# Optimization experiments

Measured on AMD Instinct MI355X. Metric: run time of the kernel, lower is better.

## Reference

```python
import jax, jax.numpy as jnp
import numpy as np
from jax.ops import segment_sum

N = 100000
E = 1600000
NFEAT, NHID, NCLS = 128, 64, 40


def setup_inputs() -> dict:
    key = jax.random.key(0)
    ks = jax.random.split(key, 8)
    x = jax.random.normal(ks[0], (N, NFEAT), dtype=jnp.float32)
    edge_index = jax.random.randint(ks[1], (2, E), 0, N, dtype=jnp.int64)
    s = lambda fi, fo: (2.0 / (fi + fo)) ** 0.5  # glorot-ish
    W1 = jax.random.normal(ks[2], (NFEAT, NHID), dtype=jnp.float32) * s(NFEAT, NHID)
    b1 = jnp.zeros((NHID,), dtype=jnp.float32)
    W2 = jax.random.normal(ks[3], (NHID, NHID), dtype=jnp.float32) * s(NHID, NHID)
    b2 = jnp.zeros((NHID,), dtype=jnp.float32)
    Wc = jax.random.normal(ks[4], (NHID, NCLS), dtype=jnp.float32) * s(NHID, NCLS)
    bc = jnp.zeros((NCLS,), dtype=jnp.float32)
    return {"x": x, "edge_index": edge_index, "W1": W1, "b1": b1,
            "W2": W2, "b2": b2, "Wc": Wc, "bc": bc}


def _gcn_conv(x, W, b, row, col, dinv):
    # x: [N, Fin] -> [N, Fout]; symmetric-normalized aggregation (PyG GCNConv)
    h = x @ W                                   # [N, Fout]
    norm = dinv[row] * dinv[col]                # [E+N]
    msg = h[row] * norm[:, None]                # [E+N, Fout]
    out = segment_sum(msg, col, num_segments=N) # [N, Fout]
    return out + b


def reference(x, edge_index, W1, b1, W2, b2, Wc, bc):
    # add self loops
    loops = jnp.arange(N, dtype=edge_index.dtype)
    row = jnp.concatenate([edge_index[0], loops])
    col = jnp.concatenate([edge_index[1], loops])
    # symmetric normalization degrees (edge weight = 1)
    deg = segment_sum(jnp.ones_like(col, dtype=x.dtype), col, num_segments=N)
    dinv = jnp.where(deg > 0, jax.lax.rsqrt(deg), 0.0)
    h = jax.nn.relu(_gcn_conv(x, W1, b1, row, col, dinv))
    h = jax.nn.relu(_gcn_conv(h, W2, b2, row, col, dinv))
    return h @ Wc + bc
```

## Files before the change

kernel.cpp:

```cpp
#include <hip/hip_runtime.h>

#define NN 100000
#define NE 1600000
#define NF 128
#define NH 64
#define NC 40

#define BKN 128
#define NBK ((NN + BKN - 1) / BKN)
#define CH  4096
#define NCHB ((NE + CH - 1) / CH)
#define CAPB 2560
#define OFFS (BKN + 1)
#define HCAP 1408
#define HTS 36

typedef short bf16x8 __attribute__((ext_vector_type(8)));
typedef float f32x4  __attribute__((ext_vector_type(4)));

__device__ __forceinline__ unsigned short f2bf(float f) {
    unsigned int u = __builtin_bit_cast(unsigned int, f);
    u += 0x7FFFu + ((u >> 16) & 1u);
    return (unsigned short)(u >> 16);
}
__device__ __forceinline__ float bfl(unsigned int u) {
    return __builtin_bit_cast(float, u << 16);
}
__device__ __forceinline__ float bfh(unsigned int u) {
    return __builtin_bit_cast(float, u & 0xFFFF0000u);
}
__device__ __forceinline__ unsigned int pk2(float a, float b) {
    return (unsigned int)f2bf(a) | ((unsigned int)f2bf(b) << 16);
}
__device__ __forceinline__ void bacc8(float4& lo, float4& hi, uint4 v) {
    lo.x += bfl(v.x); hi.x += bfh(v.x);
    lo.y += bfl(v.y); hi.y += bfh(v.y);
    lo.z += bfl(v.z); hi.z += bfh(v.z);
    lo.w += bfl(v.w); hi.w += bfh(v.w);
}

__global__ void zero_gcnt(int* __restrict__ g) {
    int i = blockIdx.x * 256 + threadIdx.x;
    if (i < NBK) g[i] = 0;
}

__global__ __launch_bounds__(256) void prep_wt(const float* __restrict__ W2,
                                               const float* __restrict__ Wc,
                                               unsigned short* __restrict__ Wt2,
                                               unsigned short* __restrict__ Wtc) {
    int t = blockIdx.x * 256 + threadIdx.x;
    if (t < 64 * 64) {
        int j = t >> 6, k = t & 63;
        Wt2[j * 64 + k] = f2bf(W2[k * 64 + j]);
    } else if (t < 64 * 64 + 48 * 64) {
        int u = t - 64 * 64;
        int j = u >> 6, k = u & 63;
        Wtc[j * 64 + k] = (j < NC) ? f2bf(Wc[k * NC + j]) : (unsigned short)0;
    }
}

__global__ __launch_bounds__(256) void bucket_scatter(const int* __restrict__ row,
                                                      const int* __restrict__ col,
                                                      int* __restrict__ gcnt,
                                                      unsigned int* __restrict__ encs) {
    __shared__ int h[NBK];
    __shared__ int loff[NBK];
    __shared__ int cur[NBK];
    __shared__ int gbase[NBK];
    __shared__ unsigned int stage[CH];
    __shared__ unsigned short sbkt[CH];
    int tid = threadIdx.x;
    for (int i = tid; i < NBK; i += 256) h[i] = 0;
    __syncthreads();
    int e0 = blockIdx.x * CH;
    int nval = NE - e0; if (nval > CH) nval = CH;
    int c[16];
    #pragma unroll
    for (int i = 0; i < 16; ++i) {
        int e = e0 + i * 256 + tid;
        c[i] = (e < NE) ? col[e] : -1;
        if (c[i] >= 0) atomicAdd(&h[c[i] >> 7], 1);
    }
    __syncthreads();
    if (tid < 64) {
        int lane = tid, base = lane * 13;
        int pre[13]; int sum = 0;
        #pragma unroll
        for (int j = 0; j < 13; ++j) {
            int idx = base + j;
            int x = (idx < NBK) ? h[idx] : 0;
            pre[j] = sum; sum += x;
        }
        int run = sum;
        #pragma unroll
        for (int d = 1; d < 64; d <<= 1) {
            int n = __shfl_up(run, d, 64);
            if (lane >= d) run += n;
        }
        int lex = run - sum;
        #pragma unroll
        for (int j = 0; j < 13; ++j) {
            int idx = base + j;
            if (idx < NBK) { loff[idx] = lex + pre[j]; cur[idx] = lex + pre[j]; }
        }
    }
    __syncthreads();
    for (int i = tid; i < NBK; i += 256) {
        int cnt = h[i];
        gbase[i] = cnt ? atomicAdd(&gcnt[i], cnt) : 0;
    }
    __syncthreads();
    #pragma unroll
    for (int i = 0; i < 16; ++i) {
        int e = e0 + i * 256 + tid;
        if (e < NE) {
            int cc = c[i], b = cc >> 7;
            int r = atomicAdd(&cur[b], 1);
            stage[r] = ((unsigned int)(cc & 127) << 24) | (unsigned int)row[e];
            sbkt[r] = (unsigned short)b;
        }
    }
    __syncthreads();
    for (int s = tid; s < nval; s += 256) {
        int b = sbkt[s];
        encs[(size_t)b * CAPB + gbase[b] + (s - loff[b])] = stage[s];
    }
}

__global__ __launch_bounds__(256) void csr_sort(unsigned int* __restrict__ encs,
                                                const int* __restrict__ gcnt,
                                                int* __restrict__ offg,
                                                float* __restrict__ dinv) {
    __shared__ unsigned int sseg[CAPB];
    __shared__ int h[BKN];
    __shared__ int off[OFFS];
    __shared__ int cur[BKN];
    int b = blockIdx.x, tid = threadIdx.x;
    if (tid < BKN) h[tid] = 0;
    __syncthreads();
    int m = gcnt[b];
    unsigned int* seg = encs + (size_t)b * CAPB;
    for (int s = tid; s < m; s += 256) {
        unsigned int e = seg[s];
        sseg[s] = e;
        atomicAdd(&h[e >> 24], 1);
    }
    __syncthreads();
    if (tid < BKN) {
        int g = b * BKN + tid;
        if (g < NN) dinv[g] = rsqrtf((float)(h[tid] + 1));
    }
    if (tid < 64) {
        int lane = tid;
        int x0 = h[lane * 2], x1 = h[lane * 2 + 1];
        int sum = x0 + x1, run = sum;
        #pragma unroll
        for (int d = 1; d < 64; d <<= 1) {
            int n = __shfl_up(run, d, 64);
            if (lane >= d) run += n;
        }
        int ex = run - sum;
        off[lane * 2] = ex;          cur[lane * 2] = ex;
        off[lane * 2 + 1] = ex + x0; cur[lane * 2 + 1] = ex + x0;
        if (lane == 63) off[BKN] = run;
    }
    __syncthreads();
    for (int s = tid; s < m; s += 256) {
        unsigned int e = sseg[s];
        int n = e >> 24;
        int r = atomicAdd(&cur[n], 1);
        seg[r] = e & 0xFFFFFFu;
    }
    if (tid < OFFS) offg[b * OFFS + tid] = off[tid];
}

template <int K, int N>
__global__ __launch_bounds__(256) void gemm_tiled(const float* __restrict__ X,
                                                  const float* __restrict__ W,
                                                  const float* __restrict__ aux,
                                                  unsigned short* __restrict__ hsb) {
    constexpr int KT  = 64;
    constexpr int KTP = KT + 4;
    __shared__ float Xl[64 * KTP];
    __shared__ float Wl[KT * N + 64];
    int tid = threadIdx.x;
    int tr = tid >> 4, tc = tid & 15;
    int rbase = blockIdx.x * 64;
    float4 acc[4] = {};

    for (int kt = 0; kt < K; kt += KT) {
        int fid = tid;
        #pragma unroll
        for (int p = 0; p < 4; ++p, fid += 256) {
            int m = fid >> 4, k4 = fid & 15;
            int rr = rbase + m; if (rr >= NN) rr = NN - 1;
            float4 v = *(const float4*)(X + (size_t)rr * K + kt + k4 * 4);
            *(float4*)(Xl + m * KTP + k4 * 4) = v;
        }
        constexpr int NW4 = KT * N / 4;
        for (int f = tid; f < NW4; f += 256)
            ((float4*)Wl)[f] = *((const float4*)(W + (size_t)kt * N) + f);
        __syncthreads();

        #pragma unroll 2
        for (int k4 = 0; k4 < KT / 4; ++k4) {
            float4 xa[4], wa[4];
            #pragma unroll
            for (int i = 0; i < 4; ++i)
                xa[i] = *(const float4*)(Xl + (tr * 4 + i) * KTP + k4 * 4);
            #pragma unroll
            for (int j = 0; j < 4; ++j)
                wa[j] = *(const float4*)(Wl + (k4 * 4 + j) * N + tc * 4);
            #pragma unroll
            for (int i = 0; i < 4; ++i) {
                acc[i].x = fmaf(xa[i].x, wa[0].x, acc[i].x);
                acc[i].y = fmaf(xa[i].x, wa[0].y, acc[i].y);
                acc[i].z = fmaf(xa[i].x, wa[0].z, acc[i].z);
                acc[i].w = fmaf(xa[i].x, wa[0].w, acc[i].w);
                acc[i].x = fmaf(xa[i].y, wa[1].x, acc[i].x);
                acc[i].y = fmaf(xa[i].y, wa[1].y, acc[i].y);
                acc[i].z = fmaf(xa[i].y, wa[1].z, acc[i].z);
                acc[i].w = fmaf(xa[i].y, wa[1].w, acc[i].w);
                acc[i].x = fmaf(xa[i].z, wa[2].x, acc[i].x);
                acc[i].y = fmaf(xa[i].z, wa[2].y, acc[i].y);
                acc[i].z = fmaf(xa[i].z, wa[2].z, acc[i].z);
                acc[i].w = fmaf(xa[i].z, wa[2].w, acc[i].w);
                acc[i].x = fmaf(xa[i].w, wa[3].x, acc[i].x);
                acc[i].y = fmaf(xa[i].w, wa[3].y, acc[i].y);
                acc[i].z = fmaf(xa[i].w, wa[3].z, acc[i].z);
                acc[i].w = fmaf(xa[i].w, wa[3].w, acc[i].w);
            }
        }
        __syncthreads();
    }

    #pragma unroll
    for (int i = 0; i < 4; ++i) {
        int r = rbase + tr * 4 + i;
        if (r < NN) {
            float d = aux[r];
            ushort4 o;
            o.x = f2bf(acc[i].x * d);
            o.y = f2bf(acc[i].y * d);
            o.z = f2bf(acc[i].z * d);
            o.w = f2bf(acc[i].w * d);
            *(ushort4*)(hsb + (size_t)r * N + tc * 4) = o;
        }
    }
}

template <int FINAL>
__global__ __launch_bounds__(256) void agg_matmul(const unsigned short* __restrict__ hs,
                                                  const int* __restrict__ srow,
                                                  const int* __restrict__ offg,
                                                  const float* __restrict__ dinv,
                                                  const float* __restrict__ biasA,
                                                  const unsigned short* __restrict__ Wt,
                                                  const float* __restrict__ biasB,
                                                  unsigned short* __restrict__ hsb_out,
                                                  float* __restrict__ f_out) {
    __shared__ int off[65];
    __shared__ int sidx[HCAP];
    __shared__ unsigned int htb[64 * HTS];
    __shared__ float sdinv[64];
    int b = blockIdx.x >> 1, half = blockIdx.x & 1;
    int tid = threadIdx.x;
    int rbase = b * BKN + half * 64;
    if (tid < 65) off[tid] = offg[b * OFFS + half * 64 + tid];
    __syncthreads();
    int e0 = off[0], cnt = off[64] - e0;
    const int* ptr = srow + (size_t)b * CAPB + e0;
    for (int s = tid; s < cnt; s += 256) sidx[s] = ptr[s];
    __syncthreads();

    int wid = tid >> 6, lane = tid & 63;
    int sg = lane >> 3, sl = lane & 7;
    const uint4* hs8 = (const uint4*)hs;
    #pragma unroll
    for (int k = 0; k < 2; ++k) {
        int n = k * 32 + wid * 8 + sg;
        int g = rbase + n;
        float d = (g < NN) ? dinv[g] : 0.f;
        if (sl == 0) sdinv[n] = d;
        float4 o0 = {}, o1 = {};
        if (g < NN) {
            float4 lo0 = {}, hi0 = {}, lo1 = {}, hi1 = {};
            float4 lo2 = {}, hi2 = {}, lo3 = {}, hi3 = {};
            bacc8(lo0, hi0, hs8[(size_t)g * 8 + sl]);
            int e = off[n] - e0, ee = off[n + 1] - e0;
            for (; e + 8 <= ee; e += 8) {
                int r0 = sidx[e + 0], r1 = sidx[e + 1];
                int r2 = sidx[e + 2], r3 = sidx[e + 3];
                int r4 = sidx[e + 4], r5 = sidx[e + 5];
                int r6 = sidx[e + 6], r7 = sidx[e + 7];
                uint4 v0 = hs8[(size_t)r0 * 8 + sl];
                uint4 v1 = hs8[(size_t)r1 * 8 + sl];
                uint4 v2 = hs8[(size_t)r2 * 8 + sl];
                uint4 v3 = hs8[(size_t)r3 * 8 + sl];
                uint4 v4 = hs8[(size_t)r4 * 8 + sl];
                uint4 v5 = hs8[(size_t)r5 * 8 + sl];
                uint4 v6 = hs8[(size_t)r6 * 8 + sl];
                uint4 v7 = hs8[(size_t)r7 * 8 + sl];
                bacc8(lo0, hi0, v0); bacc8(lo1, hi1, v1);
                bacc8(lo2, hi2, v2); bacc8(lo3, hi3, v3);
                bacc8(lo0, hi0, v4); bacc8(lo1, hi1, v5);
                bacc8(lo2, hi2, v6); bacc8(lo3, hi3, v7);
            }
            if (e + 4 <= ee) {
                int r0 = sidx[e + 0], r1 = sidx[e + 1];
                int r2 = sidx[e + 2], r3 = sidx[e + 3];
                uint4 v0 = hs8[(size_t)r0 * 8 + sl];
                uint4 v1 = hs8[(size_t)r1 * 8 + sl];
                uint4 v2 = hs8[(size_t)r2 * 8 + sl];
                uint4 v3 = hs8[(size_t)r3 * 8 + sl];
                bacc8(lo0, hi0, v0); bacc8(lo1, hi1, v1);
                bacc8(lo2, hi2, v2); bacc8(lo3, hi3, v3);
                e += 4;
            }
            for (; e < ee; ++e)
                bacc8(lo0, hi0, hs8[(size_t)sidx[e] * 8 + sl]);
            lo0.x += lo1.x + lo2.x + lo3.x;  hi0.x += hi1.x + hi2.x + hi3.x;
            lo0.y += lo1.y + lo2.y + lo3.y;  hi0.y += hi1.y + hi2.y + hi3.y;
            lo0.z += lo1.z + lo2.z + lo3.z;  hi0.z += hi1.z + hi2.z + hi3.z;
            lo0.w += lo1.w + lo2.w + lo3.w;  hi0.w += hi1.w + hi2.w + hi3.w;
            float4 bb0 = ((const float4*)biasA)[sl * 2];
            float4 bb1 = ((const float4*)biasA)[sl * 2 + 1];
            o0.x = fmaxf(fmaf(lo0.x, d, bb0.x), 0.f);
            o0.y = fmaxf(fmaf(hi0.x, d, bb0.y), 0.f);
            o0.z = fmaxf(fmaf(lo0.y, d, bb0.z), 0.f);
            o0.w = fmaxf(fmaf(hi0.y, d, bb0.w), 0.f);
            o1.x = fmaxf(fmaf(lo0.z, d, bb1.x), 0.f);
            o1.y = fmaxf(fmaf(hi0.z, d, bb1.y), 0.f);
            o1.z = fmaxf(fmaf(lo0.w, d, bb1.z), 0.f);
            o1.w = fmaxf(fmaf(hi0.w, d, bb1.w), 0.f);
        }
        uint4 pk;
        pk.x = pk2(o0.x, o0.y);
        pk.y = pk2(o0.z, o0.w);
        pk.z = pk2(o1.x, o1.y);
        pk.w = pk2(o1.z, o1.w);
        *(uint4*)&htb[n * HTS + sl * 4] = pk;
    }
    __syncthreads();

    constexpr int NCT = FINAL ? 3 : 4;
    int lm = lane & 15, lg = lane >> 4;
    bf16x8 afrag[2];
    #pragma unroll
    for (int kh = 0; kh < 2; ++kh) {
        const unsigned int* p = &htb[(wid * 16 + lm) * HTS + kh * 16 + lg * 4];
        afrag[kh] = __builtin_bit_cast(bf16x8, *(const uint4*)p);
    }
    f32x4 acc[NCT];
    #pragma unroll
    for (int ct = 0; ct < NCT; ++ct) {
        acc[ct] = (f32x4){0.f, 0.f, 0.f, 0.f};
        #pragma unroll
        for (int kh = 0; kh < 2; ++kh) {
            const unsigned short* q = Wt + (size_t)(ct * 16 + lm) * 64 + kh * 32 + lg * 8;
            bf16x8 bfrag = __builtin_bit_cast(bf16x8, *(const uint4*)q);
            acc[ct] = __builtin_amdgcn_mfma_f32_16x16x32_bf16(afrag[kh], bfrag, acc[ct], 0, 0, 0);
        }
    }

    if (!FINAL) {
        #pragma unroll
        for (int ct = 0; ct < NCT; ++ct) {
            #pragma unroll
            for (int rg = 0; rg < 4; ++rg) {
                int rloc = wid * 16 + lg * 4 + rg;
                int r = rbase + rloc;
                if (r < NN) {
                    float v = acc[ct][rg] * sdinv[rloc];
                    hsb_out[(size_t)r * NH + ct * 16 + lm] = f2bf(v);
                }
            }
        }
    } else {
        #pragma unroll
        for (int ct = 0; ct < NCT; ++ct) {
            int c = ct * 16 + lm;
            if (c < NC) {
                float bb = biasB[c];
                #pragma unroll
                for (int rg = 0; rg < 4; ++rg) {
                    int rloc = wid * 16 + lg * 4 + rg;
                    int r = rbase + rloc;
                    if (r < NN)
                        f_out[(size_t)r * NC + c] = acc[ct][rg] + bb;
                }
            }
        }
    }
}


extern "C" void kernel_launch(void* const* d_in, const int* in_sizes, int n_in,
                              void* d_out, int out_size, void* d_ws, size_t ws_size,
                              hipStream_t stream) {
    const float* x  = (const float*)d_in[0];
    const int* ei   = (const int*)d_in[1];
    const int* row  = ei;
    const int* col  = ei + NE;
    const float* W1 = (const float*)d_in[2];
    const float* b1 = (const float*)d_in[3];
    const float* W2 = (const float*)d_in[4];
    const float* b2 = (const float*)d_in[5];
    const float* Wc = (const float*)d_in[6];
    const float* bc = (const float*)d_in[7];
    float* out = (float*)d_out;

    char* ws = (char*)d_ws;
    size_t off = 0;
    auto alloc = [&](size_t bytes) {
        void* p = ws + off;
        off = (off + bytes + 255) & ~(size_t)255;
        return p;
    };
    int*   gcnt = (int*)alloc((size_t)NBK * 4);
    int*   offg = (int*)alloc((size_t)NBK * OFFS * 4);
    float* dinv = (float*)alloc((size_t)NN * 4);
    unsigned int* encs = (unsigned int*)alloc((size_t)NBK * CAPB * 4);
    unsigned short* hsb1 = (unsigned short*)alloc((size_t)NN * NH * 2);
    unsigned short* hsb2 = (unsigned short*)alloc((size_t)NN * NH * 2);
    unsigned short* Wt2  = (unsigned short*)alloc((size_t)64 * 64 * 2);
    unsigned short* Wtc  = (unsigned short*)alloc((size_t)48 * 64 * 2);

    const int GB = (NN + 63) / 64;

    zero_gcnt<<<(NBK + 255) / 256, 256, 0, stream>>>(gcnt);
    prep_wt<<<28, 256, 0, stream>>>(W2, Wc, Wt2, Wtc);
    bucket_scatter<<<NCHB, 256, 0, stream>>>(row, col, gcnt, encs);
    csr_sort<<<NBK, 256, 0, stream>>>(encs, gcnt, offg, dinv);

    gemm_tiled<NF, NH><<<GB, 256, 0, stream>>>(x, W1, dinv, hsb1);
    agg_matmul<0><<<NBK * 2, 256, 0, stream>>>(hsb1, (const int*)encs, offg, dinv,
                                               b1, Wt2, nullptr, hsb2, nullptr);
    agg_matmul<1><<<NBK * 2, 256, 0, stream>>>(hsb2, (const int*)encs, offg, dinv,
                                               b2, Wtc, bc, nullptr, out);
}
```

Measured before the change: 160.2 us.

## Use bf16 MFMA for first GEMM, widen aggregation blocks, fold zeroing into prep

Replaces the FP32 scalar-FMA tiled GEMM for layer 1 with a bf16 MFMA kernel that converts x to bf16 in shared memory and reads a pre-transposed bf16 W1. The aggregation kernels move from 256 to 512 threads so each thread handles one node/slot instead of looping twice, and the MFMA output tiles are split across 8 waves. The gcnt zeroing kernel is merged into the weight prep kernel, removing one launch. Converting x to bf16 before the first matmul lowers precision further.

After: 151.3 us. 5.6% less time.

```diff
diff --git a/kernel.cpp b/kernel.cpp
--- a/kernel.cpp
+++ b/kernel.cpp
@@ -14,6 +14,7 @@
 #define OFFS (BKN + 1)
 #define HCAP 1408
 #define HTS 36
+#define XTS 68
 
 typedef short bf16x8 __attribute__((ext_vector_type(8)));
 typedef float f32x4  __attribute__((ext_vector_type(4)));
@@ -39,23 +40,27 @@
     lo.w += bfl(v.w); hi.w += bfh(v.w);
 }
 
-__global__ void zero_gcnt(int* __restrict__ g) {
-    int i = blockIdx.x * 256 + threadIdx.x;
-    if (i < NBK) g[i] = 0;
-}
-
-__global__ __launch_bounds__(256) void prep_wt(const float* __restrict__ W2,
+__global__ __launch_bounds__(256) void prep_wt(const float* __restrict__ W1,
+                                               const float* __restrict__ W2,
                                                const float* __restrict__ Wc,
+                                               unsigned short* __restrict__ Wt1,
                                                unsigned short* __restrict__ Wt2,
-                                               unsigned short* __restrict__ Wtc) {
+                                               unsigned short* __restrict__ Wtc,
+                                               int* __restrict__ gcnt) {
     int t = blockIdx.x * 256 + threadIdx.x;
-    if (t < 64 * 64) {
-        int j = t >> 6, k = t & 63;
+    if (t < 8192) {
+        int j = t >> 7, k = t & 127;
+        Wt1[j * 128 + k] = f2bf(W1[k * 64 + j]);
+    } else if (t < 8192 + 4096) {
+        int u = t - 8192;
+        int j = u >> 6, k = u & 63;
         Wt2[j * 64 + k] = f2bf(W2[k * 64 + j]);
-    } else if (t < 64 * 64 + 48 * 64) {
-        int u = t - 64 * 64;
+    } else if (t < 8192 + 4096 + 3072) {
+        int u = t - 8192 - 4096;
         int j = u >> 6, k = u & 63;
         Wtc[j * 64 + k] = (j < NC) ? f2bf(Wc[k * NC + j]) : (unsigned short)0;
+    } else if (t < 8192 + 4096 + 3072 + NBK) {
+        gcnt[t - 8192 - 4096 - 3072] = 0;
     }
 }
 
@@ -174,83 +179,64 @@
     if (tid < OFFS) offg[b * OFFS + tid] = off[tid];
 }
 
-template <int K, int N>
-__global__ __launch_bounds__(256) void gemm_tiled(const float* __restrict__ X,
-                                                  const float* __restrict__ W,
-                                                  const float* __restrict__ aux,
+__global__ __launch_bounds__(256) void gemm1_mfma(const float* __restrict__ x,
+                                                  const unsigned short* __restrict__ Wt1,
+                                                  const float* __restrict__ dinv,
                                                   unsigned short* __restrict__ hsb) {
-    constexpr int KT  = 64;
-    constexpr int KTP = KT + 4;
-    __shared__ float Xl[64 * KTP];
-    __shared__ float Wl[KT * N + 64];
+    __shared__ unsigned int Xl[64 * XTS];
+    __shared__ float sdv[64];
     int tid = threadIdx.x;
-    int tr = tid >> 4, tc = tid & 15;
     int rbase = blockIdx.x * 64;
-    float4 acc[4] = {};
-
-    for (int kt = 0; kt < K; kt += KT) {
-        int fid = tid;
-        #pragma unroll
-        for (int p = 0; p < 4; ++p, fid += 256) {
-            int m = fid >> 4, k4 = fid & 15;
-            int rr = rbase + m; if (rr >= NN) rr = NN - 1;
-            float4 v = *(const float4*)(X + (size_t)rr * K + kt + k4 * 4);
-            *(float4*)(Xl + m * KTP + k4 * 4) = v;
-        }
-        constexpr int NW4 = KT * N / 4;
-        for (int f = tid; f < NW4; f += 256)
-            ((float4*)Wl)[f] = *((const float4*)(W + (size_t)kt * N) + f);
-        __syncthreads();
-
-        #pragma unroll 2
-        for (int k4 = 0; k4 < KT / 4; ++k4) {
-            float4 xa[4], wa[4];
-            #pragma unroll
-            for (int i = 0; i < 4; ++i)
-                xa[i] = *(const float4*)(Xl + (tr * 4 + i) * KTP + k4 * 4);
-            #pragma unroll
-            for (int j = 0; j < 4; ++j)
-                wa[j] = *(const float4*)(Wl + (k4 * 4 + j) * N + tc * 4);
-            #pragma unroll
-            for (int i = 0; i < 4; ++i) {
-                acc[i].x = fmaf(xa[i].x, wa[0].x, acc[i].x);
-                acc[i].y = fmaf(xa[i].x, wa[0].y, acc[i].y);
-                acc[i].z = fmaf(xa[i].x, wa[0].z, acc[i].z);
-                acc[i].w = fmaf(xa[i].x, wa[0].w, acc[i].w);
-                acc[i].x = fmaf(xa[i].y, wa[1].x, acc[i].x);
-                acc[i].y = fmaf(xa[i].y, wa[1].y, acc[i].y);
-                acc[i].z = fmaf(xa[i].y, wa[1].z, acc[i].z);
-                acc[i].w = fmaf(xa[i].y, wa[1].w, acc[i].w);
-                acc[i].x = fmaf(xa[i].z, wa[2].x, acc[i].x);
-                acc[i].y = fmaf(xa[i].z, wa[2].y, acc[i].y);
-                acc[i].z = fmaf(xa[i].z, wa[2].z, acc[i].z);
-                acc[i].w = fmaf(xa[i].z, wa[2].w, acc[i].w);
-                acc[i].x = fmaf(xa[i].w, wa[3].x, acc[i].x);
-                acc[i].y = fmaf(xa[i].w, wa[3].y, acc[i].y);
-                acc[i].z = fmaf(xa[i].w, wa[3].z, acc[i].z);
-                acc[i].w = fmaf(xa[i].w, wa[3].w, acc[i].w);
-            }
-        }
-        __syncthreads();
-    }
-
-    #pragma unroll
-    for (int i = 0; i < 4; ++i) {
-        int r = rbase + tr * 4 + i;
-        if (r < NN) {
-            float d = aux[r];
-            ushort4 o;
-            o.x = f2bf(acc[i].x * d);
-            o.y = f2bf(acc[i].y * d);
-            o.z = f2bf(acc[i].z * d);
-            o.w = f2bf(acc[i].w * d);
-            *(ushort4*)(hsb + (size_t)r * N + tc * 4) = o;
+    if (tid < 64) {
+        int r = rbase + tid;
+        sdv[tid] = (r < NN) ? dinv[r] : 0.f;
+    }
+    #pragma unroll
+    for (int p = 0; p < 8; ++p) {
+        int fid = p * 256 + tid;
+        int m = fid >> 5, c4 = fid & 31;
+        int rr = rbase + m; if (rr >= NN) rr = NN - 1;
+        float4 v = *(const float4*)(x + (size_t)rr * NF + c4 * 4);
+        uint2 u;
+        u.x = pk2(v.x, v.y);
+        u.y = pk2(v.z, v.w);
+        *(uint2*)&Xl[m * XTS + c4 * 2] = u;
+    }
+    __syncthreads();
+
+    int wid = tid >> 6, lane = tid & 63;
+    int lm = lane & 15, lg = lane >> 4;
+    int rt = wid;
+    bf16x8 af[4];
+    #pragma unroll
+    for (int kh = 0; kh < 4; ++kh)
+        af[kh] = __builtin_bit_cast(bf16x8,
+                    *(const uint4*)&Xl[(rt * 16 + lm) * XTS + kh * 16 + lg * 4]);
+    f32x4 acc[4];
+    #pragma unroll
+    for (int ct = 0; ct < 4; ++ct) {
+        acc[ct] = (f32x4){0.f, 0.f, 0.f, 0.f};
+        #pragma unroll
+        for (int kh = 0; kh < 4; ++kh) {
+            bf16x8 bf = __builtin_bit_cast(bf16x8,
+                *(const uint4*)(Wt1 + (size_t)(ct * 16 + lm) * 128 + kh * 32 + lg * 8));
+            acc[ct] = __builtin_amdgcn_mfma_f32_16x16x32_bf16(af[kh], bf, acc[ct], 0, 0, 0);
+        }
+    }
+    #pragma unroll
+    for (int ct = 0; ct < 4; ++ct) {
+        #pragma unroll
+        for (int rg = 0; rg < 4; ++rg) {
+            int rloc = rt * 16 + lg * 4 + rg;
+            int r = rbase + rloc;
+            if (r < NN)
+                hsb[(size_t)r * NH + ct * 16 + lm] = f2bf(acc[ct][rg] * sdv[rloc]);
         }
     }
 }
 
 template <int FINAL>
-__global__ __launch_bounds__(256) void agg_matmul(const unsigned short* __restrict__ hs,
+__global__ __launch_bounds__(512) void agg_matmul(const unsigned short* __restrict__ hs,
                                                   const int* __restrict__ srow,
                                                   const int* __restrict__ offg,
                                                   const float* __restrict__ dinv,
@@ -270,16 +256,13 @@
     __syncthreads();
     int e0 = off[0], cnt = off[64] - e0;
     const int* ptr = srow + (size_t)b * CAPB + e0;
-    for (int s = tid; s < cnt; s += 256) sidx[s] = ptr[s];
-    __syncthreads();
-
-    int wid = tid >> 6, lane = tid & 63;
-    int sg = lane >> 3, sl = lane & 7;
+    for (int s = tid; s < cnt; s += 512) sidx[s] = ptr[s];
+    __syncthreads();
+
+    int n = tid >> 3, sl = tid & 7;
+    int g = rbase + n;
     const uint4* hs8 = (const uint4*)hs;
-    #pragma unroll
-    for (int k = 0; k < 2; ++k) {
-        int n = k * 32 + wid * 8 + sg;
-        int g = rbase + n;
+    {
         float d = (g < NN) ? dinv[g] : 0.f;
         if (sl == 0) sdinv[n] = d;
         float4 o0 = {}, o1 = {};
@@ -344,50 +327,45 @@
     __syncthreads();
 
     constexpr int NCT = FINAL ? 3 : 4;
+    int wid = tid >> 6, lane = tid & 63;
     int lm = lane & 15, lg = lane >> 4;
+    int rt = wid >> 1;
+    int ct0 = (wid & 1) * 2;
+    int ct1 = (ct0 + 2 < NCT) ? ct0 + 2 : NCT;
     bf16x8 afrag[2];
     #pragma unroll
     for (int kh = 0; kh < 2; ++kh) {
-        const unsigned int* p = &htb[(wid * 16 + lm) * HTS + kh * 16 + lg * 4];
+        const unsigned int* p = &htb[(rt * 16 + lm) * HTS + kh * 16 + lg * 4];
         afrag[kh] = __builtin_bit_cast(bf16x8, *(const uint4*)p);
     }
-    f32x4 acc[NCT];
-    #pragma unroll
-    for (int ct = 0; ct < NCT; ++ct) {
-        acc[ct] = (f32x4){0.f, 0.f, 0.f, 0.f};
+    for (int ct = ct0; ct < ct1; ++ct) {
+        f32x4 acc = (f32x4){0.f, 0.f, 0.f, 0.f};
         #pragma unroll
         for (int kh = 0; kh < 2; ++kh) {
             const unsigned short* q = Wt + (size_t)(ct * 16 + lm) * 64 + kh * 32 + lg * 8;
             bf16x8 bfrag = __builtin_bit_cast(bf16x8, *(const uint4*)q);
-            acc[ct] = __builtin_amdgcn_mfma_f32_16x16x32_bf16(afrag[kh], bfrag, acc[ct], 0, 0, 0);
-        }
-    }
-
-    if (!FINAL) {
-        #pragma unroll
-        for (int ct = 0; ct < NCT; ++ct) {
+            acc = __builtin_amdgcn_mfma_f32_16x16x32_bf16(afrag[kh], bfrag, acc, 0, 0, 0);
+        }
+        if (!FINAL) {
             #pragma unroll
             for (int rg = 0; rg < 4; ++rg) {
-                int rloc = wid * 16 + lg * 4 + rg;
+                int rloc = rt * 16 + lg * 4 + rg;
                 int r = rbase + rloc;
                 if (r < NN) {
-                    float v = acc[ct][rg] * sdinv[rloc];
+                    float v = acc[rg] * sdinv[rloc];
                     hsb_out[(size_t)r * NH + ct * 16 + lm] = f2bf(v);
                 }
             }
-        }
-    } else {
-        #pragma unroll
-        for (int ct = 0; ct < NCT; ++ct) {
+        } else {
             int c = ct * 16 + lm;
             if (c < NC) {
                 float bb = biasB[c];
                 #pragma unroll
                 for (int rg = 0; rg < 4; ++rg) {
-                    int rloc = wid * 16 + lg * 4 + rg;
+                    int rloc = rt * 16 + lg * 4 + rg;
                     int r = rbase + rloc;
                     if (r < NN)
-                        f_out[(size_t)r * NC + c] = acc[ct][rg] + bb;
+                        f_out[(size_t)r * NC + c] = acc[rg] + bb;
                 }
             }
         }
@@ -423,19 +401,19 @@
     unsigned int* encs = (unsigned int*)alloc((size_t)NBK * CAPB * 4);
     unsigned short* hsb1 = (unsigned short*)alloc((size_t)NN * NH * 2);
     unsigned short* hsb2 = (unsigned short*)alloc((size_t)NN * NH * 2);
+    unsigned short* Wt1  = (unsigned short*)alloc((size_t)64 * 128 * 2);
     unsigned short* Wt2  = (unsigned short*)alloc((size_t)64 * 64 * 2);
     unsigned short* Wtc  = (unsigned short*)alloc((size_t)48 * 64 * 2);
 
     const int GB = (NN + 63) / 64;
 
-    zero_gcnt<<<(NBK + 255) / 256, 256, 0, stream>>>(gcnt);
-    prep_wt<<<28, 256, 0, stream>>>(W2, Wc, Wt2, Wtc);
+    prep_wt<<<64, 256, 0, stream>>>(W1, W2, Wc, Wt1, Wt2, Wtc, gcnt);
     bucket_scatter<<<NCHB, 256, 0, stream>>>(row, col, gcnt, encs);
     csr_sort<<<NBK, 256, 0, stream>>>(encs, gcnt, offg, dinv);
 
-    gemm_tiled<NF, NH><<<GB, 256, 0, stream>>>(x, W1, dinv, hsb1);
-    agg_matmul<0><<<NBK * 2, 256, 0, stream>>>(hsb1, (const int*)encs, offg, dinv,
+    gemm1_mfma<<<GB, 256, 0, stream>>>(x, Wt1, dinv, hsb1);
+    agg_matmul<0><<<NBK * 2, 512, 0, stream>>>(hsb1, (const int*)encs, offg, dinv,
                                                b1, Wt2, nullptr, hsb2, nullptr);
-    agg_matmul<1><<<NBK * 2, 256, 0, stream>>>(hsb2, (const int*)encs, offg, dinv,
+    agg_matmul<1><<<NBK * 2, 512, 0, stream>>>(hsb2, (const int*)encs, offg, dinv,
                                                b2, Wtc, bc, nullptr, out);
 }
```
